# Performance work log

Hardware: AMD Instinct MI355X
Metric: run time of the kernel (lower is better)

Reference implementation:

```python
import jax, jax.numpy as jnp
import numpy as np
import itertools

B, N, K, G = 1024, 1024, 6, 720  # G = K!
H1, H2, C = 64, 32, 40
IN = K * 3


def setup_inputs() -> dict:
    key = jax.random.key(0)
    ks = jax.random.split(key, 8)
    x = jax.random.normal(ks[0], (B, N, 3), dtype=jnp.float32)
    # per-sample subsample indices (torch uses randperm(N)[:K]; distinctness
    # is irrelevant to the math, randint keeps them in-range)
    idx = jax.random.randint(ks[1], (B, K), 0, N)
    perms = jnp.asarray(
        np.array(list(itertools.permutations(range(K))), dtype=np.int32)
    )  # (G, K)
    # MLP params: torch Linear default init ~ U(-1/sqrt(fan_in), 1/sqrt(fan_in))
    def lin(k, fin, fout):
        kw, kb = jax.random.split(k)
        s = 1.0 / np.sqrt(fin)
        W = jax.random.uniform(kw, (fin, fout), jnp.float32, -s, s)
        b = jax.random.uniform(kb, (fout,), jnp.float32, -s, s)
        return W, b
    W1, b1 = lin(ks[2], IN, H1)
    W2, b2 = lin(ks[3], H1, H2)
    W3, b3 = lin(ks[4], H2, C)
    return dict(x=x, W1=W1, b1=b1, W2=W2, b2=b2, W3=W3, b3=b3,
                idx=idx, perms=perms)


def reference(x, W1, b1, W2, b2, W3, b3, idx, perms):
    Bv = x.shape[0]
    Gv, Kv = perms.shape
    # gather the K subsampled points per batch element: (B, K, 3)
    pts = jnp.take_along_axis(x, idx[:, :, None], axis=1)
    # expand over all K! permutations of the point ordering: (B, G, K, 3)
    permuted = pts[:, perms, :]
    flat = permuted.reshape(Bv, Gv, Kv * 3)  # (B, G, K*3)
    h = jax.nn.relu(flat @ W1 + b1)          # (B, G, H1)
    h = jax.nn.relu(h @ W2 + b2)             # (B, G, H2)
    y = h @ W3 + b3                          # (B, G, C)
    return y.mean(axis=1)                    # (B, C)
```

## Files before the change

### kernel.cpp

```cpp
#include <hip/hip_runtime.h>
#include <hip/hip_bf16.h>

typedef __attribute__((ext_vector_type(8))) short short8;
typedef __attribute__((ext_vector_type(4))) float f32x4;
typedef unsigned int u32;
typedef __attribute__((ext_vector_type(4))) unsigned int u32x4;

#define NN 1024

#define LFENCE { asm volatile("s_waitcnt lgkmcnt(0)" ::: "memory"); __builtin_amdgcn_sched_barrier(0); }

#define PAIR_W(BUF, R2, TA, TB) { \
  float va_ = fmaxf(bx_ + (TA), 0.0f), vb_ = fmaxf(bx_ + (TB), 0.0f); \
  u32 pk_; asm("v_cvt_pk_bf16_f32 %0, %1, %2" : "=v"(pk_) : "v"(va_), "v"(vb_)); \
  BUF[(R2)*64 + (lane ^ ((((R2)) & 7) << 3))] = pk_; \
}

#define ROWP3(BUF, R2B, BX) { const float bx_ = (BX); \
  PAIR_W(BUF,(R2B)+0, T0_, T1_) PAIR_W(BUF,(R2B)+1, T2_, T3_) PAIR_W(BUF,(R2B)+2, T4_, T5_) }

#define SGR(BUF, A0,A1,A2, M0,M1,M2) do { \
  const float f0_ = b1v + P[(A0)*6+0]; \
  const float f1_ = b1v + P[(A1)*6+0]; \
  const float f2_ = b1v + P[(A2)*6+0]; \
  const float g12_ = P[(A1)*6+1] + P[(A2)*6+2]; \
  const float g21_ = P[(A2)*6+1] + P[(A1)*6+2]; \
  const float g02_ = P[(A0)*6+1] + P[(A2)*6+2]; \
  const float g20_ = P[(A2)*6+1] + P[(A0)*6+2]; \
  const float g01_ = P[(A0)*6+1] + P[(A1)*6+2]; \
  const float g10_ = P[(A1)*6+1] + P[(A0)*6+2]; \
  const float e0_ = P[(M0)*6+3], e1_ = P[(M1)*6+3], e2_ = P[(M2)*6+3]; \
  const float h12_ = P[(M1)*6+4] + P[(M2)*6+5]; \
  const float h21_ = P[(M2)*6+4] + P[(M1)*6+5]; \
  const float h02_ = P[(M0)*6+4] + P[(M2)*6+5]; \
  const float h20_ = P[(M2)*6+4] + P[(M0)*6+5]; \
  const float h01_ = P[(M0)*6+4] + P[(M1)*6+5]; \
  const float h10_ = P[(M1)*6+4] + P[(M0)*6+5]; \
  const float T0_ = e0_+h12_, T1_ = e0_+h21_, T2_ = e1_+h02_; \
  const float T3_ = e1_+h20_, T4_ = e2_+h01_, T5_ = e2_+h10_; \
  const float B0_ = f0_+g12_, B1_ = f0_+g21_, B2_ = f1_+g02_; \
  const float B3_ = f1_+g20_, B4_ = f2_+g01_, B5_ = f2_+g10_; \
  ROWP3(BUF, 0,  B0_) ROWP3(BUF, 3,  B1_) ROWP3(BUF, 6,  B2_) \
  ROWP3(BUF, 9,  B3_) ROWP3(BUF, 12, B4_) ROWP3(BUF, 15, B5_) \
} while(0)

#define MFMA4T(A0_, A1_) do { \
  f32x4 c0_ = {b2v0,b2v0,b2v0,b2v0}; \
  f32x4 c1_ = {b2v1,b2v1,b2v1,b2v1}; \
  c0_ = __builtin_amdgcn_mfma_f32_16x16x32_bf16(A0_, bh00, c0_, 0,0,0); \
  c0_ = __builtin_amdgcn_mfma_f32_16x16x32_bf16(A1_, bh10, c0_, 0,0,0); \
  c1_ = __builtin_amdgcn_mfma_f32_16x16x32_bf16(A0_, bh01, c1_, 0,0,0); \
  c1_ = __builtin_amdgcn_mfma_f32_16x16x32_bf16(A1_, bh11, c1_, 0,0,0); \
  acc0[0]+=fmaxf(c0_[0],0.f); acc0[1]+=fmaxf(c0_[1],0.f); \
  acc0[2]+=fmaxf(c0_[2],0.f); acc0[3]+=fmaxf(c0_[3],0.f); \
  acc1[0]+=fmaxf(c1_[0],0.f); acc1[1]+=fmaxf(c1_[1],0.f); \
  acc1[2]+=fmaxf(c1_[2],0.f); acc1[3]+=fmaxf(c1_[3],0.f); \
} while(0)

#define READQ(BUF) { \
  q0  = *(const u32x4*)&BUF[e0b];         q1  = *(const u32x4*)&BUF[e0b+4]; \
  q2  = *(const u32x4*)&BUF[e1b];         q3  = *(const u32x4*)&BUF[e1b+4]; \
  q4  = *(const u32x4*)&BUF[512+e0b];     q5  = *(const u32x4*)&BUF[512+e0b+4]; \
  q6  = *(const u32x4*)&BUF[512+e1b];     q7  = *(const u32x4*)&BUF[512+e1b+4]; \
  q8  = *(const u32x4*)&BUF[1024+e0b];    q9  = *(const u32x4*)&BUF[1024+e0b+4]; \
  q10 = *(const u32x4*)&BUF[1024+e1b];    q11 = *(const u32x4*)&BUF[1024+e1b+4]; }

#define FRAG(dst, qa_, qb_) { \
  u32x4 t_; \
  t_[0] = __builtin_amdgcn_perm(qa_[1], qa_[0], sel); \
  t_[1] = __builtin_amdgcn_perm(qa_[3], qa_[2], sel); \
  t_[2] = __builtin_amdgcn_perm(qb_[1], qb_[0], sel); \
  t_[3] = __builtin_amdgcn_perm(qb_[3], qb_[2], sel); \
  dst = __builtin_bit_cast(short8, t_); }

#define MFMA3 { \
  short8 A0_, A1_; \
  FRAG(A0_, q0, q1);   FRAG(A1_, q2, q3);   MFMA4T(A0_, A1_); \
  FRAG(A0_, q4, q5);   FRAG(A1_, q6, q7);   MFMA4T(A0_, A1_); \
  FRAG(A0_, q8, q9);   FRAG(A1_, q10, q11); MFMA4T(A0_, A1_); }

#define CHUNK(BUF, A0,A1,A2, M0,M1,M2) { SGR(BUF, A0,A1,A2, M0,M1,M2); READQ(BUF); LFENCE; }

#define ALLCHUNKS \
    if (wv == 0) { \
        CHUNK(wb0, 0,1,2, 3,4,5); \
        MFMA3; CHUNK(wb1, 0,1,3, 2,4,5); \
        MFMA3; CHUNK(wb0, 0,1,4, 2,3,5); \
        MFMA3; CHUNK(wb1, 0,1,5, 2,3,4); \
        MFMA3; CHUNK(wb0, 0,2,3, 1,4,5); \
        MFMA3; \
    } else if (wv == 1) { \
        CHUNK(wb0, 0,2,4, 1,3,5); \
        MFMA3; CHUNK(wb1, 0,2,5, 1,3,4); \
        MFMA3; CHUNK(wb0, 0,3,4, 1,2,5); \
        MFMA3; CHUNK(wb1, 0,3,5, 1,2,4); \
        MFMA3; CHUNK(wb0, 0,4,5, 1,2,3); \
        MFMA3; \
    } else if (wv == 2) { \
        CHUNK(wb0, 1,2,3, 0,4,5); \
        MFMA3; CHUNK(wb1, 1,2,4, 0,3,5); \
        MFMA3; CHUNK(wb0, 1,2,5, 0,3,4); \
        MFMA3; CHUNK(wb1, 1,3,4, 0,2,5); \
        MFMA3; CHUNK(wb0, 1,3,5, 0,2,4); \
        MFMA3; \
    } else { \
        CHUNK(wb0, 1,4,5, 0,2,3); \
        MFMA3; CHUNK(wb1, 2,3,4, 0,1,5); \
        MFMA3; CHUNK(wb0, 2,3,5, 0,1,4); \
        MFMA3; CHUNK(wb1, 2,4,5, 0,1,3); \
        MFMA3; CHUNK(wb0, 3,4,5, 0,1,2); \
        MFMA3; \
    }

#define MKB(dst_h, KH, NIDX) do { \
  _Pragma("unroll") \
  for (int e_ = 0; e_ < 8; ++e_) { \
    float f_ = W2[((KH)*32 + kg*8 + e_)*32 + 16*(NIDX) + colb]; \
    __hip_bfloat16 hi_ = __float2bfloat16(f_); \
    dst_h[e_] = *(short*)&hi_; \
  } \
} while(0)

__global__ __launch_bounds__(256, 2) void symm_mlp_kernel(
    const float* __restrict__ x,
    const float* __restrict__ W1, const float* __restrict__ b1,
    const float* __restrict__ W2, const float* __restrict__ b2,
    const float* __restrict__ W3, const float* __restrict__ b3,
    const int* __restrict__ idx,
    float* __restrict__ out)
{
    __shared__ u32 h1s[4][2][24 * 64];
    __shared__ float redbuf[4][32];

    const int tid   = threadIdx.x;
    const int lane  = tid & 63;
    const int wv    = tid >> 6;
    const int batch = blockIdx.x;

    int pidx[6];
    #pragma unroll
    for (int k = 0; k < 6; ++k) pidx[k] = idx[batch * 6 + k];

    float px[6][3];
    #pragma unroll
    for (int k = 0; k < 6; ++k)
        #pragma unroll
        for (int d = 0; d < 3; ++d) px[k][d] = x[(batch * NN + pidx[k]) * 3 + d];

    float w1c[18];
    #pragma unroll
    for (int r = 0; r < 18; ++r) w1c[r] = W1[r * 64 + lane];

    const float b1v = b1[lane];
    const int colb = lane & 15, kg = lane >> 4;
    const float b2v0 = b2[colb];
    const float b2v1 = b2[16 + colb];

    short8 bh00, bh10, bh01, bh11;
    MKB(bh00, 0, 0);
    MKB(bh10, 1, 0);
    MKB(bh01, 0, 1);
    MKB(bh11, 1, 1);

    float P[36];
    #pragma unroll
    for (int k = 0; k < 6; ++k)
    #pragma unroll
    for (int j = 0; j < 6; ++j)
        P[k*6+j] = fmaf(px[k][2], w1c[3*j+2], fmaf(px[k][1], w1c[3*j+1], px[k][0] * w1c[3*j+0]));

    u32* wb0 = &h1s[wv][0][0];
    u32* wb1 = &h1s[wv][1][0];
    #pragma unroll
    for (int r2p = 18; r2p < 24; ++r2p) { wb0[r2p*64 + lane] = 0u; wb1[r2p*64 + lane] = 0u; }

    const int r2l = (lane & 15) >> 1;
    const int sm  = r2l << 3;
    const int e0b = r2l * 64 + ((kg * 8) ^ sm);
    const int e1b = r2l * 64 + ((32 + kg * 8) ^ sm);
    const u32 sel = (lane & 1) ? 0x07060302u : 0x05040100u;

    f32x4 acc0 = {0.f,0.f,0.f,0.f}, acc1 = {0.f,0.f,0.f,0.f};
    u32x4 q0,q1,q2,q3,q4,q5,q6,q7,q8,q9,q10,q11;

    ALLCHUNKS

    float s0 = acc0[0] + acc0[1] + acc0[2] + acc0[3];
    float s1 = acc1[0] + acc1[1] + acc1[2] + acc1[3];
    s0 += __shfl_xor(s0, 16, 64);  s0 += __shfl_xor(s0, 32, 64);
    s1 += __shfl_xor(s1, 16, 64);  s1 += __shfl_xor(s1, 32, 64);
    s0 -= 60.0f * fmaxf(b2v0, 0.0f);
    s1 -= 60.0f * fmaxf(b2v1, 0.0f);

    if (lane < 16)       redbuf[wv][lane] = s0;
    else if (lane < 32)  redbuf[wv][lane] = s1;
    __syncthreads();

    if (tid < 40) {
        float m[32];
        #pragma unroll
        for (int c = 0; c < 32; ++c)
            m[c] = (redbuf[0][c] + redbuf[1][c] + redbuf[2][c] + redbuf[3][c]) * (1.0f / 720.0f);
        float y = b3[tid];
        #pragma unroll
        for (int c = 0; c < 32; ++c) y = fmaf(m[c], W3[c * 40 + tid], y);
        out[batch * 40 + tid] = y;
    }
}

extern "C" void kernel_launch(void* const* d_in, const int* in_sizes, int n_in,
                              void* d_out, int out_size, void* d_ws, size_t ws_size,
                              hipStream_t stream) {
    const float* x  = (const float*)d_in[0];
    const float* W1 = (const float*)d_in[1];
    const float* b1 = (const float*)d_in[2];
    const float* W2 = (const float*)d_in[3];
    const float* b2 = (const float*)d_in[4];
    const float* W3 = (const float*)d_in[5];
    const float* b3 = (const float*)d_in[6];
    const int* idx   = (const int*)d_in[7];
    float* out = (float*)d_out;

    symm_mlp_kernel<<<1024, 256, 0, stream>>>(x, W1, b1, W2, b2, W3, b3, idx, out);
}
```

Measured before the change: 19.05 us.

## Replace per-wave unrolled chunk branches with a table-driven rolled loop

The four fully unrolled per-wave branches become one rolled loop over five chunks. Each chunk's point-subset indices come from a constant table, and the gathered points are held in scalar registers via readfirstlane. The 36-entry precomputed P array is dropped, so projections are recomputed per chunk from the selected points, and the LDS double buffer shrinks to a single buffer. The aim is to cut code size, instruction-cache pressure and VGPR/LDS use, at the cost of extra per-chunk ALU work and the loss of overlap between the next chunk's writes and the current chunk's MFMAs.

```diff
diff --git a/kernel.cpp b/kernel.cpp
--- a/kernel.cpp
+++ b/kernel.cpp
@@ -10,39 +10,34 @@
 
 #define LFENCE { asm volatile("s_waitcnt lgkmcnt(0)" ::: "memory"); __builtin_amdgcn_sched_barrier(0); }
 
-#define PAIR_W(BUF, R2, TA, TB) { \
+#define PK3(a,b,c) ((u32)(a) | ((u32)(b)<<8) | ((u32)(c)<<16))
+__constant__ u32 sgtab[20][2] = {
+  {PK3(0,1,2), PK3(3,4,5)}, {PK3(0,1,3), PK3(2,4,5)}, {PK3(0,1,4), PK3(2,3,5)},
+  {PK3(0,1,5), PK3(2,3,4)}, {PK3(0,2,3), PK3(1,4,5)},
+  {PK3(0,2,4), PK3(1,3,5)}, {PK3(0,2,5), PK3(1,3,4)}, {PK3(0,3,4), PK3(1,2,5)},
+  {PK3(0,3,5), PK3(1,2,4)}, {PK3(0,4,5), PK3(1,2,3)},
+  {PK3(1,2,3), PK3(0,4,5)}, {PK3(1,2,4), PK3(0,3,5)}, {PK3(1,2,5), PK3(0,3,4)},
+  {PK3(1,3,4), PK3(0,2,5)}, {PK3(1,3,5), PK3(0,2,4)},
+  {PK3(1,4,5), PK3(0,2,3)}, {PK3(2,3,4), PK3(0,1,5)}, {PK3(2,3,5), PK3(0,1,4)},
+  {PK3(2,4,5), PK3(0,1,3)}, {PK3(3,4,5), PK3(0,1,2)},
+};
+
+__device__ __forceinline__ float rflf(float v) {
+    return __int_as_float(__builtin_amdgcn_readfirstlane(__float_as_int(v)));
+}
+
+#define SEL6(I, V0,V1,V2,V3,V4,V5) \
+  ((I)==0?(V0):(I)==1?(V1):(I)==2?(V2):(I)==3?(V3):(I)==4?(V4):(V5))
+
+#define DOT3(PX,PY,PZ,J) fmaf((PZ), w1c[3*(J)+2], fmaf((PY), w1c[3*(J)+1], (PX)*w1c[3*(J)]))
+
+#define PAIR_W(R2, TA, TB) { \
   float va_ = fmaxf(bx_ + (TA), 0.0f), vb_ = fmaxf(bx_ + (TB), 0.0f); \
   u32 pk_; asm("v_cvt_pk_bf16_f32 %0, %1, %2" : "=v"(pk_) : "v"(va_), "v"(vb_)); \
-  BUF[(R2)*64 + (lane ^ ((((R2)) & 7) << 3))] = pk_; \
-}
-
-#define ROWP3(BUF, R2B, BX) { const float bx_ = (BX); \
-  PAIR_W(BUF,(R2B)+0, T0_, T1_) PAIR_W(BUF,(R2B)+1, T2_, T3_) PAIR_W(BUF,(R2B)+2, T4_, T5_) }
-
-#define SGR(BUF, A0,A1,A2, M0,M1,M2) do { \
-  const float f0_ = b1v + P[(A0)*6+0]; \
-  const float f1_ = b1v + P[(A1)*6+0]; \
-  const float f2_ = b1v + P[(A2)*6+0]; \
-  const float g12_ = P[(A1)*6+1] + P[(A2)*6+2]; \
-  const float g21_ = P[(A2)*6+1] + P[(A1)*6+2]; \
-  const float g02_ = P[(A0)*6+1] + P[(A2)*6+2]; \
-  const float g20_ = P[(A2)*6+1] + P[(A0)*6+2]; \
-  const float g01_ = P[(A0)*6+1] + P[(A1)*6+2]; \
-  const float g10_ = P[(A1)*6+1] + P[(A0)*6+2]; \
-  const float e0_ = P[(M0)*6+3], e1_ = P[(M1)*6+3], e2_ = P[(M2)*6+3]; \
-  const float h12_ = P[(M1)*6+4] + P[(M2)*6+5]; \
-  const float h21_ = P[(M2)*6+4] + P[(M1)*6+5]; \
-  const float h02_ = P[(M0)*6+4] + P[(M2)*6+5]; \
-  const float h20_ = P[(M2)*6+4] + P[(M0)*6+5]; \
-  const float h01_ = P[(M0)*6+4] + P[(M1)*6+5]; \
-  const float h10_ = P[(M1)*6+4] + P[(M0)*6+5]; \
-  const float T0_ = e0_+h12_, T1_ = e0_+h21_, T2_ = e1_+h02_; \
-  const float T3_ = e1_+h20_, T4_ = e2_+h01_, T5_ = e2_+h10_; \
-  const float B0_ = f0_+g12_, B1_ = f0_+g21_, B2_ = f1_+g02_; \
-  const float B3_ = f1_+g20_, B4_ = f2_+g01_, B5_ = f2_+g10_; \
-  ROWP3(BUF, 0,  B0_) ROWP3(BUF, 3,  B1_) ROWP3(BUF, 6,  B2_) \
-  ROWP3(BUF, 9,  B3_) ROWP3(BUF, 12, B4_) ROWP3(BUF, 15, B5_) \
-} while(0)
+  wb[(R2)*64 + (lane ^ ((((R2)) & 7) << 3))] = pk_; \
+}
+#define ROWP3(R2B, BX) { const float bx_ = (BX); \
+  PAIR_W((R2B)+0, T0, T1) PAIR_W((R2B)+1, T2, T3) PAIR_W((R2B)+2, T4, T5) }
 
 #define MFMA4T(A0_, A1_) do { \
   f32x4 c0_ = {b2v0,b2v0,b2v0,b2v0}; \
@@ -57,13 +52,13 @@
   acc1[2]+=fmaxf(c1_[2],0.f); acc1[3]+=fmaxf(c1_[3],0.f); \
 } while(0)
 
-#define READQ(BUF) { \
-  q0  = *(const u32x4*)&BUF[e0b];         q1  = *(const u32x4*)&BUF[e0b+4]; \
-  q2  = *(const u32x4*)&BUF[e1b];         q3  = *(const u32x4*)&BUF[e1b+4]; \
-  q4  = *(const u32x4*)&BUF[512+e0b];     q5  = *(const u32x4*)&BUF[512+e0b+4]; \
-  q6  = *(const u32x4*)&BUF[512+e1b];     q7  = *(const u32x4*)&BUF[512+e1b+4]; \
-  q8  = *(const u32x4*)&BUF[1024+e0b];    q9  = *(const u32x4*)&BUF[1024+e0b+4]; \
-  q10 = *(const u32x4*)&BUF[1024+e1b];    q11 = *(const u32x4*)&BUF[1024+e1b+4]; }
+#define READQ { \
+  q0  = *(const u32x4*)&wb[e0b];         q1  = *(const u32x4*)&wb[e0b+4]; \
+  q2  = *(const u32x4*)&wb[e1b];         q3  = *(const u32x4*)&wb[e1b+4]; \
+  q4  = *(const u32x4*)&wb[512+e0b];     q5  = *(const u32x4*)&wb[512+e0b+4]; \
+  q6  = *(const u32x4*)&wb[512+e1b];     q7  = *(const u32x4*)&wb[512+e1b+4]; \
+  q8  = *(const u32x4*)&wb[1024+e0b];    q9  = *(const u32x4*)&wb[1024+e0b+4]; \
+  q10 = *(const u32x4*)&wb[1024+e1b];    q11 = *(const u32x4*)&wb[1024+e1b+4]; }
 
 #define FRAG(dst, qa_, qb_) { \
   u32x4 t_; \
@@ -74,43 +69,10 @@
   dst = __builtin_bit_cast(short8, t_); }
 
 #define MFMA3 { \
-  short8 A0_, A1_; \
-  FRAG(A0_, q0, q1);   FRAG(A1_, q2, q3);   MFMA4T(A0_, A1_); \
-  FRAG(A0_, q4, q5);   FRAG(A1_, q6, q7);   MFMA4T(A0_, A1_); \
-  FRAG(A0_, q8, q9);   FRAG(A1_, q10, q11); MFMA4T(A0_, A1_); }
-
-#define CHUNK(BUF, A0,A1,A2, M0,M1,M2) { SGR(BUF, A0,A1,A2, M0,M1,M2); READQ(BUF); LFENCE; }
-
-#define ALLCHUNKS \
-    if (wv == 0) { \
-        CHUNK(wb0, 0,1,2, 3,4,5); \
-        MFMA3; CHUNK(wb1, 0,1,3, 2,4,5); \
-        MFMA3; CHUNK(wb0, 0,1,4, 2,3,5); \
-        MFMA3; CHUNK(wb1, 0,1,5, 2,3,4); \
-        MFMA3; CHUNK(wb0, 0,2,3, 1,4,5); \
-        MFMA3; \
-    } else if (wv == 1) { \
-        CHUNK(wb0, 0,2,4, 1,3,5); \
-        MFMA3; CHUNK(wb1, 0,2,5, 1,3,4); \
-        MFMA3; CHUNK(wb0, 0,3,4, 1,2,5); \
-        MFMA3; CHUNK(wb1, 0,3,5, 1,2,4); \
-        MFMA3; CHUNK(wb0, 0,4,5, 1,2,3); \
-        MFMA3; \
-    } else if (wv == 2) { \
-        CHUNK(wb0, 1,2,3, 0,4,5); \
-        MFMA3; CHUNK(wb1, 1,2,4, 0,3,5); \
-        MFMA3; CHUNK(wb0, 1,2,5, 0,3,4); \
-        MFMA3; CHUNK(wb1, 1,3,4, 0,2,5); \
-        MFMA3; CHUNK(wb0, 1,3,5, 0,2,4); \
-        MFMA3; \
-    } else { \
-        CHUNK(wb0, 1,4,5, 0,2,3); \
-        MFMA3; CHUNK(wb1, 2,3,4, 0,1,5); \
-        MFMA3; CHUNK(wb0, 2,3,5, 0,1,4); \
-        MFMA3; CHUNK(wb1, 2,4,5, 0,1,3); \
-        MFMA3; CHUNK(wb0, 3,4,5, 0,1,2); \
-        MFMA3; \
-    }
+  short8 A0f_, A1f_; \
+  FRAG(A0f_, q0, q1);   FRAG(A1f_, q2, q3);   MFMA4T(A0f_, A1f_); \
+  FRAG(A0f_, q4, q5);   FRAG(A1f_, q6, q7);   MFMA4T(A0f_, A1f_); \
+  FRAG(A0f_, q8, q9);   FRAG(A1f_, q10, q11); MFMA4T(A0f_, A1f_); }
 
 #define MKB(dst_h, KH, NIDX) do { \
   _Pragma("unroll") \
@@ -129,23 +91,27 @@
     const int* __restrict__ idx,
     float* __restrict__ out)
 {
-    __shared__ u32 h1s[4][2][24 * 64];
+    __shared__ u32 h1s[4][24 * 64];
     __shared__ float redbuf[4][32];
 
     const int tid   = threadIdx.x;
     const int lane  = tid & 63;
     const int wv    = tid >> 6;
+    const int wvs   = __builtin_amdgcn_readfirstlane(tid) >> 6;
     const int batch = blockIdx.x;
 
-    int pidx[6];
-    #pragma unroll
-    for (int k = 0; k < 6; ++k) pidx[k] = idx[batch * 6 + k];
-
-    float px[6][3];
-    #pragma unroll
-    for (int k = 0; k < 6; ++k)
-        #pragma unroll
-        for (int d = 0; d < 3; ++d) px[k][d] = x[(batch * NN + pidx[k]) * 3 + d];
+    const int p0 = __builtin_amdgcn_readfirstlane(idx[batch*6+0]);
+    const int p1 = __builtin_amdgcn_readfirstlane(idx[batch*6+1]);
+    const int p2 = __builtin_amdgcn_readfirstlane(idx[batch*6+2]);
+    const int p3 = __builtin_amdgcn_readfirstlane(idx[batch*6+3]);
+    const int p4 = __builtin_amdgcn_readfirstlane(idx[batch*6+4]);
+    const int p5 = __builtin_amdgcn_readfirstlane(idx[batch*6+5]);
+    const float sx0 = rflf(x[(batch*NN+p0)*3+0]), sy0 = rflf(x[(batch*NN+p0)*3+1]), sz0 = rflf(x[(batch*NN+p0)*3+2]);
+    const float sx1 = rflf(x[(batch*NN+p1)*3+0]), sy1 = rflf(x[(batch*NN+p1)*3+1]), sz1 = rflf(x[(batch*NN+p1)*3+2]);
+    const float sx2 = rflf(x[(batch*NN+p2)*3+0]), sy2 = rflf(x[(batch*NN+p2)*3+1]), sz2 = rflf(x[(batch*NN+p2)*3+2]);
+    const float sx3 = rflf(x[(batch*NN+p3)*3+0]), sy3 = rflf(x[(batch*NN+p3)*3+1]), sz3 = rflf(x[(batch*NN+p3)*3+2]);
+    const float sx4 = rflf(x[(batch*NN+p4)*3+0]), sy4 = rflf(x[(batch*NN+p4)*3+1]), sz4 = rflf(x[(batch*NN+p4)*3+2]);
+    const float sx5 = rflf(x[(batch*NN+p5)*3+0]), sy5 = rflf(x[(batch*NN+p5)*3+1]), sz5 = rflf(x[(batch*NN+p5)*3+2]);
 
     float w1c[18];
     #pragma unroll
@@ -162,17 +128,9 @@
     MKB(bh01, 0, 1);
     MKB(bh11, 1, 1);
 
-    float P[36];
+    u32* wb = &h1s[wv][0];
     #pragma unroll
-    for (int k = 0; k < 6; ++k)
-    #pragma unroll
-    for (int j = 0; j < 6; ++j)
-        P[k*6+j] = fmaf(px[k][2], w1c[3*j+2], fmaf(px[k][1], w1c[3*j+1], px[k][0] * w1c[3*j+0]));
-
-    u32* wb0 = &h1s[wv][0][0];
-    u32* wb1 = &h1s[wv][1][0];
-    #pragma unroll
-    for (int r2p = 18; r2p < 24; ++r2p) { wb0[r2p*64 + lane] = 0u; wb1[r2p*64 + lane] = 0u; }
+    for (int r2p = 18; r2p < 24; ++r2p) wb[r2p*64 + lane] = 0u;
 
     const int r2l = (lane & 15) >> 1;
     const int sm  = r2l << 3;
@@ -183,7 +141,46 @@
     f32x4 acc0 = {0.f,0.f,0.f,0.f}, acc1 = {0.f,0.f,0.f,0.f};
     u32x4 q0,q1,q2,q3,q4,q5,q6,q7,q8,q9,q10,q11;
 
-    ALLCHUNKS
+    #pragma unroll 1
+    for (int c = 0; c < 5; ++c) {
+        const u32 tx = sgtab[wvs*5 + c][0];
+        const u32 ty = sgtab[wvs*5 + c][1];
+        const int A0 = tx & 255, A1 = (tx >> 8) & 255, A2 = (tx >> 16) & 255;
+        const int M0 = ty & 255, M1 = (ty >> 8) & 255, M2 = (ty >> 16) & 255;
+
+        const float ax0 = SEL6(A0,sx0,sx1,sx2,sx3,sx4,sx5), ay0 = SEL6(A0,sy0,sy1,sy2,sy3,sy4,sy5), az0 = SEL6(A0,sz0,sz1,sz2,sz3,sz4,sz5);
+        const float ax1 = SEL6(A1,sx0,sx1,sx2,sx3,sx4,sx5), ay1 = SEL6(A1,sy0,sy1,sy2,sy3,sy4,sy5), az1 = SEL6(A1,sz0,sz1,sz2,sz3,sz4,sz5);
+        const float ax2 = SEL6(A2,sx0,sx1,sx2,sx3,sx4,sx5), ay2 = SEL6(A2,sy0,sy1,sy2,sy3,sy4,sy5), az2 = SEL6(A2,sz0,sz1,sz2,sz3,sz4,sz5);
+        const float mx0 = SEL6(M0,sx0,sx1,sx2,sx3,sx4,sx5), my0 = SEL6(M0,sy0,sy1,sy2,sy3,sy4,sy5), mz0 = SEL6(M0,sz0,sz1,sz2,sz3,sz4,sz5);
+        const float mx1 = SEL6(M1,sx0,sx1,sx2,sx3,sx4,sx5), my1 = SEL6(M1,sy0,sy1,sy2,sy3,sy4,sy5), mz1 = SEL6(M1,sz0,sz1,sz2,sz3,sz4,sz5);
+        const float mx2 = SEL6(M2,sx0,sx1,sx2,sx3,sx4,sx5), my2 = SEL6(M2,sy0,sy1,sy2,sy3,sy4,sy5), mz2 = SEL6(M2,sz0,sz1,sz2,sz3,sz4,sz5);
+
+        const float a0s0 = DOT3(ax0,ay0,az0,0), a0s1 = DOT3(ax0,ay0,az0,1), a0s2 = DOT3(ax0,ay0,az0,2);
+        const float a1s0 = DOT3(ax1,ay1,az1,0), a1s1 = DOT3(ax1,ay1,az1,1), a1s2 = DOT3(ax1,ay1,az1,2);
+        const float a2s0 = DOT3(ax2,ay2,az2,0), a2s1 = DOT3(ax2,ay2,az2,1), a2s2 = DOT3(ax2,ay2,az2,2);
+        const float m0s3 = DOT3(mx0,my0,mz0,3), m0s4 = DOT3(mx0,my0,mz0,4), m0s5 = DOT3(mx0,my0,mz0,5);
+        const float m1s3 = DOT3(mx1,my1,mz1,3), m1s4 = DOT3(mx1,my1,mz1,4), m1s5 = DOT3(mx1,my1,mz1,5);
+        const float m2s3 = DOT3(mx2,my2,mz2,3), m2s4 = DOT3(mx2,my2,mz2,4), m2s5 = DOT3(mx2,my2,mz2,5);
+
+        const float f0 = b1v + a0s0, f1 = b1v + a1s0, f2 = b1v + a2s0;
+        const float g12 = a1s1 + a2s2, g21 = a2s1 + a1s2;
+        const float g02 = a0s1 + a2s2, g20 = a2s1 + a0s2;
+        const float g01 = a0s1 + a1s2, g10 = a1s1 + a0s2;
+        const float h12 = m1s4 + m2s5, h21 = m2s4 + m1s5;
+        const float h02 = m0s4 + m2s5, h20 = m2s4 + m0s5;
+        const float h01 = m0s4 + m1s5, h10 = m1s4 + m0s5;
+        const float T0 = m0s3 + h12, T1 = m0s3 + h21, T2 = m1s3 + h02;
+        const float T3 = m1s3 + h20, T4 = m2s3 + h01, T5 = m2s3 + h10;
+        const float B0 = f0 + g12, B1 = f0 + g21, B2 = f1 + g02;
+        const float B3 = f1 + g20, B4 = f2 + g01, B5 = f2 + g10;
+
+        ROWP3(0,  B0) ROWP3(3,  B1) ROWP3(6,  B2)
+        ROWP3(9,  B3) ROWP3(12, B4) ROWP3(15, B5)
+
+        READQ;
+        LFENCE;
+        MFMA3;
+    }
 
     float s0 = acc0[0] + acc0[1] + acc0[2] + acc0[3];
     float s1 = acc1[0] + acc1[1] + acc1[2] + acc1[3];
```

New measurement: 23.41 us. 1.23x slower.

## Pack four permutation chunks densely into one LDS buffer to cut padding rows

Applied to the files above, without the earlier changes.

Each wave now writes four 18-row chunks contiguously into a single 72-row LDS region instead of double-buffering 24-row padded chunks. It then runs the MFMA passes over 16-row tiles with no padding, so only the fifth chunk needs 6 zero-padding rows, and the bias correction drops from 60 to 12 padded rows. The goal is to remove wasted MFMA work on zero rows (20 tiles become 16) and to batch LDS writes with precomputed per-row XOR pointers. In exchange, compute and write no longer overlap across chunks, so the kernel gives up the double-buffered pipelining, and the larger LDS footprint could limit occupancy.

```diff
diff --git a/kernel.cpp b/kernel.cpp
--- a/kernel.cpp
+++ b/kernel.cpp
@@ -10,16 +10,14 @@
 
 #define LFENCE { asm volatile("s_waitcnt lgkmcnt(0)" ::: "memory"); __builtin_amdgcn_sched_barrier(0); }
 
-#define PAIR_W(BUF, R2, TA, TB) { \
+#define PKROW(DST, TA, TB) { \
   float va_ = fmaxf(bx_ + (TA), 0.0f), vb_ = fmaxf(bx_ + (TB), 0.0f); \
-  u32 pk_; asm("v_cvt_pk_bf16_f32 %0, %1, %2" : "=v"(pk_) : "v"(va_), "v"(vb_)); \
-  BUF[(R2)*64 + (lane ^ ((((R2)) & 7) << 3))] = pk_; \
-}
-
-#define ROWP3(BUF, R2B, BX) { const float bx_ = (BX); \
-  PAIR_W(BUF,(R2B)+0, T0_, T1_) PAIR_W(BUF,(R2B)+1, T2_, T3_) PAIR_W(BUF,(R2B)+2, T4_, T5_) }
-
-#define SGR(BUF, A0,A1,A2, M0,M1,M2) do { \
+  asm("v_cvt_pk_bf16_f32 %0, %1, %2" : "=v"(DST) : "v"(va_), "v"(vb_)); }
+
+#define PK3(KA,KB,KC, BX) { const float bx_ = (BX); \
+  PKROW(KA, T0_, T1_) PKROW(KB, T2_, T3_) PKROW(KC, T4_, T5_) }
+
+#define SGCOMP(A0,A1,A2, M0,M1,M2) { \
   const float f0_ = b1v + P[(A0)*6+0]; \
   const float f1_ = b1v + P[(A1)*6+0]; \
   const float f2_ = b1v + P[(A2)*6+0]; \
@@ -38,11 +36,23 @@
   const float h10_ = P[(M1)*6+4] + P[(M0)*6+5]; \
   const float T0_ = e0_+h12_, T1_ = e0_+h21_, T2_ = e1_+h02_; \
   const float T3_ = e1_+h20_, T4_ = e2_+h01_, T5_ = e2_+h10_; \
-  const float B0_ = f0_+g12_, B1_ = f0_+g21_, B2_ = f1_+g02_; \
-  const float B3_ = f1_+g20_, B4_ = f2_+g01_, B5_ = f2_+g10_; \
-  ROWP3(BUF, 0,  B0_) ROWP3(BUF, 3,  B1_) ROWP3(BUF, 6,  B2_) \
-  ROWP3(BUF, 9,  B3_) ROWP3(BUF, 12, B4_) ROWP3(BUF, 15, B5_) \
-} while(0)
+  PK3(k0,k1,k2,   f0_+g12_)  PK3(k3,k4,k5,   f0_+g21_) \
+  PK3(k6,k7,k8,   f1_+g02_)  PK3(k9,k10,k11, f1_+g20_) \
+  PK3(k12,k13,k14,f2_+g01_)  PK3(k15,k16,k17,f2_+g10_) }
+
+#define WRT16(BB) { \
+  bp0[(BB+0)*64]=k0;  bp0[(BB+8)*64]=k8;  \
+  bp1[(BB+1)*64]=k1;  bp1[(BB+9)*64]=k9;  \
+  bp2[(BB+2)*64]=k2;  bp2[(BB+10)*64]=k10; \
+  bp3[(BB+3)*64]=k3;  bp3[(BB+11)*64]=k11; \
+  bp4[(BB+4)*64]=k4;  bp4[(BB+12)*64]=k12; \
+  bp5[(BB+5)*64]=k5;  bp5[(BB+13)*64]=k13; \
+  bp6[(BB+6)*64]=k6;  bp6[(BB+14)*64]=k14; \
+  bp7[(BB+7)*64]=k7;  bp7[(BB+15)*64]=k15; }
+
+#define WOV(RA, RB) { \
+  wb[(RA)*64 + (lane ^ ((((RA)) & 7) << 3))] = k16; \
+  wb[(RB)*64 + (lane ^ ((((RB)) & 7) << 3))] = k17; }
 
 #define MFMA4T(A0_, A1_) do { \
   f32x4 c0_ = {b2v0,b2v0,b2v0,b2v0}; \
@@ -57,13 +67,13 @@
   acc1[2]+=fmaxf(c1_[2],0.f); acc1[3]+=fmaxf(c1_[3],0.f); \
 } while(0)
 
-#define READQ(BUF) { \
-  q0  = *(const u32x4*)&BUF[e0b];         q1  = *(const u32x4*)&BUF[e0b+4]; \
-  q2  = *(const u32x4*)&BUF[e1b];         q3  = *(const u32x4*)&BUF[e1b+4]; \
-  q4  = *(const u32x4*)&BUF[512+e0b];     q5  = *(const u32x4*)&BUF[512+e0b+4]; \
-  q6  = *(const u32x4*)&BUF[512+e1b];     q7  = *(const u32x4*)&BUF[512+e1b+4]; \
-  q8  = *(const u32x4*)&BUF[1024+e0b];    q9  = *(const u32x4*)&BUF[1024+e0b+4]; \
-  q10 = *(const u32x4*)&BUF[1024+e1b];    q11 = *(const u32x4*)&BUF[1024+e1b+4]; }
+#define RQ(B) { \
+  q0  = *(const u32x4*)&wb[(B)+e0b];       q1  = *(const u32x4*)&wb[(B)+e0b+4]; \
+  q2  = *(const u32x4*)&wb[(B)+e1b];       q3  = *(const u32x4*)&wb[(B)+e1b+4]; \
+  q4  = *(const u32x4*)&wb[(B)+512+e0b];   q5  = *(const u32x4*)&wb[(B)+512+e0b+4]; \
+  q6  = *(const u32x4*)&wb[(B)+512+e1b];   q7  = *(const u32x4*)&wb[(B)+512+e1b+4]; \
+  q8  = *(const u32x4*)&wb[(B)+1024+e0b];  q9  = *(const u32x4*)&wb[(B)+1024+e0b+4]; \
+  q10 = *(const u32x4*)&wb[(B)+1024+e1b];  q11 = *(const u32x4*)&wb[(B)+1024+e1b+4]; }
 
 #define FRAG(dst, qa_, qb_) { \
   u32x4 t_; \
@@ -73,44 +83,15 @@
   t_[3] = __builtin_amdgcn_perm(qb_[3], qb_[2], sel); \
   dst = __builtin_bit_cast(short8, t_); }
 
-#define MFMA3 { \
-  short8 A0_, A1_; \
-  FRAG(A0_, q0, q1);   FRAG(A1_, q2, q3);   MFMA4T(A0_, A1_); \
-  FRAG(A0_, q4, q5);   FRAG(A1_, q6, q7);   MFMA4T(A0_, A1_); \
-  FRAG(A0_, q8, q9);   FRAG(A1_, q10, q11); MFMA4T(A0_, A1_); }
-
-#define CHUNK(BUF, A0,A1,A2, M0,M1,M2) { SGR(BUF, A0,A1,A2, M0,M1,M2); READQ(BUF); LFENCE; }
-
-#define ALLCHUNKS \
-    if (wv == 0) { \
-        CHUNK(wb0, 0,1,2, 3,4,5); \
-        MFMA3; CHUNK(wb1, 0,1,3, 2,4,5); \
-        MFMA3; CHUNK(wb0, 0,1,4, 2,3,5); \
-        MFMA3; CHUNK(wb1, 0,1,5, 2,3,4); \
-        MFMA3; CHUNK(wb0, 0,2,3, 1,4,5); \
-        MFMA3; \
-    } else if (wv == 1) { \
-        CHUNK(wb0, 0,2,4, 1,3,5); \
-        MFMA3; CHUNK(wb1, 0,2,5, 1,3,4); \
-        MFMA3; CHUNK(wb0, 0,3,4, 1,2,5); \
-        MFMA3; CHUNK(wb1, 0,3,5, 1,2,4); \
-        MFMA3; CHUNK(wb0, 0,4,5, 1,2,3); \
-        MFMA3; \
-    } else if (wv == 2) { \
-        CHUNK(wb0, 1,2,3, 0,4,5); \
-        MFMA3; CHUNK(wb1, 1,2,4, 0,3,5); \
-        MFMA3; CHUNK(wb0, 1,2,5, 0,3,4); \
-        MFMA3; CHUNK(wb1, 1,3,4, 0,2,5); \
-        MFMA3; CHUNK(wb0, 1,3,5, 0,2,4); \
-        MFMA3; \
-    } else { \
-        CHUNK(wb0, 1,4,5, 0,2,3); \
-        MFMA3; CHUNK(wb1, 2,3,4, 0,1,5); \
-        MFMA3; CHUNK(wb0, 2,3,5, 0,1,4); \
-        MFMA3; CHUNK(wb1, 2,4,5, 0,1,3); \
-        MFMA3; CHUNK(wb0, 3,4,5, 0,1,2); \
-        MFMA3; \
-    }
+#define M3 { \
+  short8 A0f_, A1f_; \
+  FRAG(A0f_, q0, q1);   FRAG(A1f_, q2, q3);   MFMA4T(A0f_, A1f_); \
+  FRAG(A0f_, q4, q5);   FRAG(A1f_, q6, q7);   MFMA4T(A0f_, A1f_); \
+  FRAG(A0f_, q8, q9);   FRAG(A1f_, q10, q11); MFMA4T(A0f_, A1f_); }
+
+#define ZPAD6 { \
+  wb[18*64+(lane^16)]=0u; wb[19*64+(lane^24)]=0u; wb[20*64+(lane^32)]=0u; \
+  wb[21*64+(lane^40)]=0u; wb[22*64+(lane^48)]=0u; wb[23*64+(lane^56)]=0u; }
 
 #define MKB(dst_h, KH, NIDX) do { \
   _Pragma("unroll") \
@@ -129,7 +110,7 @@
     const int* __restrict__ idx,
     float* __restrict__ out)
 {
-    __shared__ u32 h1s[4][2][24 * 64];
+    __shared__ u32 h1s[4][72 * 64];
     __shared__ float redbuf[4][32];
 
     const int tid   = threadIdx.x;
@@ -169,10 +150,15 @@
     for (int j = 0; j < 6; ++j)
         P[k*6+j] = fmaf(px[k][2], w1c[3*j+2], fmaf(px[k][1], w1c[3*j+1], px[k][0] * w1c[3*j+0]));
 
-    u32* wb0 = &h1s[wv][0][0];
-    u32* wb1 = &h1s[wv][1][0];
-    #pragma unroll
-    for (int r2p = 18; r2p < 24; ++r2p) { wb0[r2p*64 + lane] = 0u; wb1[r2p*64 + lane] = 0u; }
+    u32* wb  = &h1s[wv][0];
+    u32* bp0 = wb + (lane ^ 0);
+    u32* bp1 = wb + (lane ^ 8);
+    u32* bp2 = wb + (lane ^ 16);
+    u32* bp3 = wb + (lane ^ 24);
+    u32* bp4 = wb + (lane ^ 32);
+    u32* bp5 = wb + (lane ^ 40);
+    u32* bp6 = wb + (lane ^ 48);
+    u32* bp7 = wb + (lane ^ 56);
 
     const int r2l = (lane & 15) >> 1;
     const int sm  = r2l << 3;
@@ -182,15 +168,47 @@
 
     f32x4 acc0 = {0.f,0.f,0.f,0.f}, acc1 = {0.f,0.f,0.f,0.f};
     u32x4 q0,q1,q2,q3,q4,q5,q6,q7,q8,q9,q10,q11;
-
-    ALLCHUNKS
+    u32 k0,k1,k2,k3,k4,k5,k6,k7,k8,k9,k10,k11,k12,k13,k14,k15,k16,k17;
+
+    if (wv == 0) {
+        SGCOMP(0,1,2, 3,4,5); WRT16(0);  WOV(64,65);
+        SGCOMP(0,1,3, 2,4,5); WRT16(16); WOV(66,67);
+        SGCOMP(0,1,4, 2,3,5); WRT16(32); WOV(68,69);
+        SGCOMP(0,1,5, 2,3,4); WRT16(48); WOV(70,71);
+    } else if (wv == 1) {
+        SGCOMP(0,2,4, 1,3,5); WRT16(0);  WOV(64,65);
+        SGCOMP(0,2,5, 1,3,4); WRT16(16); WOV(66,67);
+        SGCOMP(0,3,4, 1,2,5); WRT16(32); WOV(68,69);
+        SGCOMP(0,3,5, 1,2,4); WRT16(48); WOV(70,71);
+    } else if (wv == 2) {
+        SGCOMP(1,2,3, 0,4,5); WRT16(0);  WOV(64,65);
+        SGCOMP(1,2,4, 0,3,5); WRT16(16); WOV(66,67);
+        SGCOMP(1,2,5, 0,3,4); WRT16(32); WOV(68,69);
+        SGCOMP(1,3,4, 0,2,5); WRT16(48); WOV(70,71);
+    } else {
+        SGCOMP(1,4,5, 0,2,3); WRT16(0);  WOV(64,65);
+        SGCOMP(2,3,4, 0,1,5); WRT16(16); WOV(66,67);
+        SGCOMP(2,3,5, 0,1,4); WRT16(32); WOV(68,69);
+        SGCOMP(2,4,5, 0,1,3); WRT16(48); WOV(70,71);
+    }
+    RQ(0);    LFENCE; M3;
+    RQ(1536);         M3;
+    RQ(3072);         M3;
+
+    ZPAD6;
+    if (wv == 0)      { SGCOMP(0,2,3, 1,4,5); }
+    else if (wv == 1) { SGCOMP(0,4,5, 1,2,3); }
+    else if (wv == 2) { SGCOMP(1,3,5, 0,2,4); }
+    else              { SGCOMP(3,4,5, 0,1,2); }
+    WRT16(0); WOV(16,17);
+    RQ(0); LFENCE; M3;
 
     float s0 = acc0[0] + acc0[1] + acc0[2] + acc0[3];
     float s1 = acc1[0] + acc1[1] + acc1[2] + acc1[3];
     s0 += __shfl_xor(s0, 16, 64);  s0 += __shfl_xor(s0, 32, 64);
     s1 += __shfl_xor(s1, 16, 64);  s1 += __shfl_xor(s1, 32, 64);
-    s0 -= 60.0f * fmaxf(b2v0, 0.0f);
-    s1 -= 60.0f * fmaxf(b2v1, 0.0f);
+    s0 -= 12.0f * fmaxf(b2v0, 0.0f);
+    s1 -= 12.0f * fmaxf(b2v1, 0.0f);
 
     if (lane < 16)       redbuf[wv][lane] = s0;
     else if (lane < 32)  redbuf[wv][lane] = s1;
```

New measurement: 18.98 us. No clear change (-0.4%).
